# Kernel tuning notes

Hardware: AMD Instinct MI355X
Metric: run time of the kernel (lower is better)

Reference implementation:

```python
import jax, jax.numpy as jnp
import numpy as np

DECAY = 0.99
EPSILON = 1e-05
COMMITMENT_COST = 0.25
N_TOKENS = 8192   # B * h * w = 8 * 32 * 32
EMBED_DIM = 4096
VOCAB = 8192


def setup_inputs() -> dict:
    key = jax.random.key(0)
    k1, k2, k3 = jax.random.split(key, 3)
    return {
        "inputs": jax.random.normal(k1, (N_TOKENS, EMBED_DIM), dtype=jnp.float32),
        "embedding": jax.random.normal(k2, (VOCAB, EMBED_DIM), dtype=jnp.float32),
        "ema_w": jax.random.normal(k3, (VOCAB, EMBED_DIM), dtype=jnp.float32),
        "ema_cluster_size": jnp.zeros((VOCAB,), dtype=jnp.float32),
    }


def reference(inputs, embedding, ema_w, ema_cluster_size):
    n_tokens = inputs.shape[0]
    vocab = embedding.shape[0]
    distances = (jnp.sum(inputs * inputs, axis=1, keepdims=True)
                 + jnp.sum(embedding * embedding, axis=1)
                 - 2.0 * jnp.matmul(inputs, embedding.T))
    encoding_indices = jnp.argmin(distances, axis=1)            # [N]
    # one-hot @ embedding == gather of codebook rows
    quantized = embedding[encoding_indices]                      # [N, D]
    # sum of one-hot encodings over tokens == per-code counts
    counts = jax.ops.segment_sum(jnp.ones((n_tokens,), inputs.dtype),
                                 encoding_indices, num_segments=vocab)  # [V]
    # EMA cluster-size update with Laplace smoothing
    new_cluster_size = ema_cluster_size * DECAY + (1.0 - DECAY) * counts
    n = jnp.sum(new_cluster_size)
    new_cluster_size = (new_cluster_size + EPSILON) / (n + vocab * EPSILON) * n
    # dw = encodings.T @ flat_input == scatter-add of inputs per code
    dw = jax.ops.segment_sum(inputs, encoding_indices, num_segments=vocab)  # [V, D]
    new_ema_w = ema_w * DECAY + (1.0 - DECAY) * dw
    new_embedding = new_ema_w / new_cluster_size[:, None]
    # commitment loss (codebook side detached)
    e_latent_loss = jnp.mean((jax.lax.stop_gradient(quantized) - inputs) ** 2)
    loss = COMMITMENT_COST * e_latent_loss
    # straight-through estimator
    quantized_st = inputs + jax.lax.stop_gradient(quantized - inputs)
    avg_probs = counts / n_tokens
    perplexity = jnp.exp(-jnp.sum(avg_probs * jnp.log(avg_probs + 1e-10)))
    return (loss, quantized_st, perplexity, encoding_indices[:, None],
            new_cluster_size, new_ema_w, new_embedding)
```

## Files before the change

kernel.cpp:

```cpp
#include <hip/hip_runtime.h>
#include <hip/hip_fp16.h>
#include <stdint.h>

typedef _Float16 f16;
typedef float f32x4 __attribute__((ext_vector_type(4)));
typedef unsigned long long u64;
typedef long long i64;
typedef long long i64x2 __attribute__((ext_vector_type(2)));

#define N_TOK 8192
#define VOCAB 8192
#define DIM   4096
#define DELTA 64.0f

__device__ __forceinline__ void gload16(const void* g, void* l) {
    __builtin_amdgcn_global_load_lds(
        (const __attribute__((address_space(1))) unsigned int*)(uintptr_t)g,
        (__attribute__((address_space(3))) unsigned int*)(uintptr_t)l,
        16, 0, 0);
}

__device__ __forceinline__ float keyinv(unsigned k) {
    unsigned b = (k & 0x80000000u) ? (k ^ 0x80000000u) : ~k;
    return __uint_as_float(b);
}

__device__ __forceinline__ void ins2(u64& k1, u64& k2, u64 v) {
    if (v < k1) { k2 = k1; k1 = v; }
    else if (v < k2) { k2 = v; }
}

__global__ __launch_bounds__(256) void k_pack(const float* __restrict__ inputs,
                                              const float* __restrict__ embedding,
                                              char* __restrict__ apk, char* __restrict__ bpk,
                                              float* __restrict__ enorms,
                                              int* __restrict__ counts) {
    int b = blockIdx.x, t = threadIdx.x;
    bool isB = b >= N_TOK;
    int row = isB ? b - N_TOK : b;
    const float* src = (isB ? embedding : inputs) + (size_t)row * DIM;
    char* dst = (isB ? bpk : apk) + (size_t)row * DIM;
    double nrm = 0.0;
#pragma unroll
    for (int k = 0; k < 4; k++) {
        int d0 = t * 4 + 1024 * k;
        float4 v = *(const float4*)(src + d0);
        nrm += (double)v.x * v.x + (double)v.y * v.y
             + (double)v.z * v.z + (double)v.w * v.w;
        int packed = 0;
        packed = __builtin_amdgcn_cvt_pk_fp8_f32(v.x, v.y, packed, false);
        packed = __builtin_amdgcn_cvt_pk_fp8_f32(v.z, v.w, packed, true);
        int c = d0 & 127;
        int s8 = c >> 3, kk = s8 >> 2, g = s8 & 3;
        int q8 = ((kk & 2) << 2) | (g << 1) | (kk & 1);
        *(int*)(dst + (d0 & ~127) + (q8 << 3) + (c & 7)) = packed;
    }
    if (isB) {
        __shared__ double red[256];
        red[t] = nrm;
        __syncthreads();
        for (int off = 128; off > 0; off >>= 1) {
            if (t < off) red[t] += red[t + off];
            __syncthreads();
        }
        if (t == 0) {
            enorms[row] = (float)red[0];
            counts[row] = 0;
        }
    }
}

__global__ __launch_bounds__(512) void k_gemm(const char* __restrict__ apk,
                                              const char* __restrict__ bpk,
                                              const float* __restrict__ enorms,
                                              u64* __restrict__ cand) {
    extern __shared__ char lds[];
    int b = blockIdx.x;
    int x = b & 7, l = b >> 3;
    int bm = x * 4 + ((l >> 3) & 3);
    int bn = (l >> 5) * 8 + (l & 7);
    int tid = threadIdx.x;
    int lane = tid & 63, wid = tid >> 6;
    int wm = wid >> 2, wn = wid & 3;

    const char* srcs[8];
    unsigned lof[8];
#pragma unroll
    for (int e = 0; e < 8; e++) {
        int tile = e >> 2, q = e & 3;
        int s = q * 512 + tid;
        int r = s >> 3;
        int c16 = (s & 7) ^ (r & 7);
        int row = (tile ? bn : bm) * 256 + r;
        srcs[e] = (tile ? bpk : apk) + (size_t)row * DIM + c16 * 16;
        lof[e] = tile * 32768 + q * 8192 + wid * 1024;
    }

    f32x4 acc[8][4];
#pragma unroll
    for (int m = 0; m < 8; m++)
#pragma unroll
        for (int n = 0; n < 4; n++) acc[m][n] = (f32x4){0.f, 0.f, 0.f, 0.f};

    const int g = lane >> 4;
    const int ra = wm * 128 + (lane & 15);
    const int rb = wn * 64 + (lane & 15);

#define STAGE(buf) { _Pragma("unroll") for (int e = 0; e < 8; e++) { \
        gload16(srcs[e], &lds[(buf) * 65536u + lof[e]]); srcs[e] += 128; } }

    STAGE(0);

    for (int kt = 0; kt < 32; ++kt) {
        const unsigned cur = (kt & 1) ? 65536u : 0u;
        if (kt < 31) {
            STAGE((kt & 1) ^ 1);
            asm volatile("s_waitcnt vmcnt(8)" ::: "memory");
        } else {
            asm volatile("s_waitcnt vmcnt(0)" ::: "memory");
        }
        __builtin_amdgcn_sched_barrier(0);
        __builtin_amdgcn_s_barrier();
        __builtin_amdgcn_s_setprio(1);
#pragma unroll
        for (int h = 0; h < 2; h++) {
            i64x2 bv[4];
#pragma unroll
            for (int n = 0; n < 4; n++) {
                int r = rb + n * 16;
                bv[n] = *(const i64x2*)&lds[cur + 32768 + r * 128 + ((((h << 2) + g) ^ (r & 7)) << 4)];
            }
#pragma unroll
            for (int m = 0; m < 8; m++) {
                int r = ra + m * 16;
                i64x2 av = *(const i64x2*)&lds[cur + r * 128 + ((((h << 2) + g) ^ (r & 7)) << 4)];
#pragma unroll
                for (int n = 0; n < 4; n++) {
                    acc[m][n] = __builtin_amdgcn_mfma_f32_16x16x32_fp8_fp8(av[0], bv[n][0], acc[m][n], 0, 0, 0);
                    acc[m][n] = __builtin_amdgcn_mfma_f32_16x16x32_fp8_fp8(av[1], bv[n][1], acc[m][n], 0, 0, 0);
                }
            }
        }
        __builtin_amdgcn_s_setprio(0);
        __builtin_amdgcn_s_barrier();
    }
#undef STAGE

    float en[4];
    int colb = bn * 256 + wn * 64 + (lane & 15);
#pragma unroll
    for (int n = 0; n < 4; n++) en[n] = enorms[colb + n * 16];
#pragma unroll
    for (int m = 0; m < 8; m++) {
#pragma unroll
        for (int reg = 0; reg < 4; reg++) {
            u64 k1 = ~0ull, k2 = ~0ull;
#pragma unroll
            for (int n = 0; n < 4; n++) {
                float d = en[n] - 2.0f * acc[m][n][reg];
                unsigned bb = __float_as_uint(d);
                unsigned key = (bb & 0x80000000u) ? ~bb : (bb | 0x80000000u);
                ins2(k1, k2, ((u64)key << 32) | (unsigned)(colb + n * 16));
            }
#pragma unroll
            for (int msk = 1; msk < 16; msk <<= 1) {
                u64 o1 = __shfl_xor(k1, msk, 64);
                u64 o2 = __shfl_xor(k2, msk, 64);
                ins2(k1, k2, o1);
                ins2(k1, k2, o2);
            }
            if ((lane & 15) == 0) {
                int rowg = bm * 256 + wm * 128 + m * 16 + ((lane >> 4) << 2) + reg;
                size_t slot = ((size_t)rowg * 32 + bn) * 4 + wn;
                ulonglong2 v; v.x = k1; v.y = k2;
                *(ulonglong2*)&cand[slot * 2] = v;
            }
        }
    }
}

__global__ __launch_bounds__(256) void k_cand(const u64* __restrict__ cand,
                                              const float* __restrict__ enorms,
                                              const float* __restrict__ inputs,
                                              const float* __restrict__ embedding,
                                              float* __restrict__ o_idx,
                                              float* __restrict__ o_quant,
                                              float* __restrict__ partials,
                                              int* __restrict__ counts) {
    int tok = blockIdx.x, t = threadIdx.x;
    int lane = t & 63, w = t >> 6;
    __shared__ u64 redu[4];
    __shared__ float redf[4];
    __shared__ float pdot[64][4];
    __shared__ int clist[64];
    __shared__ int s_cnt;
    if (t == 0) s_cnt = 0;
    u64 e = cand[(size_t)tok * 256 + t];
    u64 v = e;
#pragma unroll
    for (int msk = 1; msk < 64; msk <<= 1) {
        u64 o = __shfl_xor(v, msk, 64);
        if (o < v) v = o;
    }
    if (lane == 0) redu[w] = v;
    __syncthreads();
    u64 m01 = redu[0] < redu[1] ? redu[0] : redu[1];
    u64 m23 = redu[2] < redu[3] ? redu[2] : redu[3];
    u64 mall = m01 < m23 ? m01 : m23;
    float dmin = keyinv((unsigned)(mall >> 32));
    float myd = keyinv((unsigned)(e >> 32));
    if (myd <= dmin + DELTA) {
        int p = atomicAdd(&s_cnt, 1);
        if (p < 64) clist[p] = (int)(unsigned)(e & 0xffffffffu);
    }
    __syncthreads();
    int nc = min(s_cnt, 64);

    const float* xrow = inputs + (size_t)tok * DIM;
    float4 xr4[4];
#pragma unroll
    for (int k = 0; k < 4; k++) xr4[k] = *(const float4*)(xrow + t * 4 + 1024 * k);

    for (int i = 0; i < nc; i++) {
        int c = clist[i];
        const float* erow = embedding + (size_t)c * DIM;
        float p = 0.f;
#pragma unroll
        for (int k = 0; k < 4; k++) {
            float4 e4 = *(const float4*)(erow + t * 4 + 1024 * k);
            p += xr4[k].x * e4.x + xr4[k].y * e4.y + xr4[k].z * e4.z + xr4[k].w * e4.w;
        }
#pragma unroll
        for (int msk = 1; msk < 64; msk <<= 1) p += __shfl_xor(p, msk, 64);
        if (lane == 0) pdot[i][w] = p;
    }
    __syncthreads();

    float best = 3.4e38f;
    int bcol = 0x7fffffff;
    for (int i = 0; i < nc; i++) {
        int c = clist[i];
        float dot = (pdot[i][0] + pdot[i][1]) + (pdot[i][2] + pdot[i][3]);
        float dist = enorms[c] - 2.0f * dot;
        if (dist < best || (dist == best && c < bcol)) { best = dist; bcol = c; }
    }
    const float* eb = embedding + (size_t)bcol * DIM;
    float* qrow = o_quant + (size_t)tok * DIM;
    float ls = 0.f;
#pragma unroll
    for (int k = 0; k < 4; k++) {
        int d = t * 4 + 1024 * k;
        float4 q4 = *(const float4*)(eb + d);
        qrow[d + 0] = q4.x; qrow[d + 1] = q4.y; qrow[d + 2] = q4.z; qrow[d + 3] = q4.w;
        float dx = q4.x - xr4[k].x, dy = q4.y - xr4[k].y;
        float dz = q4.z - xr4[k].z, dw = q4.w - xr4[k].w;
        ls += dx * dx + dy * dy + dz * dz + dw * dw;
    }
#pragma unroll
    for (int msk = 1; msk < 64; msk <<= 1) ls += __shfl_xor(ls, msk, 64);
    if (lane == 0) redf[w] = ls;
    __syncthreads();
    if (t == 0) {
        partials[tok] = (redf[0] + redf[1]) + (redf[2] + redf[3]);
        o_idx[tok] = (float)bcol;
        atomicAdd(&counts[bcol], 1);
    }
}

__global__ __launch_bounds__(1024) void k_cs(const int* __restrict__ counts,
                                             const float* __restrict__ ema_cs,
                                             float* __restrict__ o_ncs,
                                             float* __restrict__ o_perp) {
    __shared__ float red[1024];
    int t = threadIdx.x;
    float pre[8];
    float psum = 0.f, esum = 0.f;
#pragma unroll
    for (int k = 0; k < 8; k++) {
        int j = t * 8 + k;
        float c = (float)counts[j];
        float p = ema_cs[j] * 0.99f + 0.01f * c;
        pre[k] = p;
        psum += p;
        float ap = c * (1.0f / 8192.0f);
        esum += ap * logf(ap + 1e-10f);
    }
    red[t] = psum;
    __syncthreads();
    for (int off = 512; off > 0; off >>= 1) {
        if (t < off) red[t] += red[t + off];
        __syncthreads();
    }
    float n = red[0];
    __syncthreads();
    red[t] = esum;
    __syncthreads();
    for (int off = 512; off > 0; off >>= 1) {
        if (t < off) red[t] += red[t + off];
        __syncthreads();
    }
    if (t == 0) o_perp[0] = expf(-red[0]);
    float scale = n / (n + (float)VOCAB * 1e-5f);
#pragma unroll
    for (int k = 0; k < 8; k++) {
        int j = t * 8 + k;
        o_ncs[j] = (pre[k] + 1e-5f) * scale;
    }
}

__global__ __launch_bounds__(1024) void k_loss(const float* __restrict__ partials,
                                               float* __restrict__ o_loss) {
    __shared__ float red[1024];
    int t = threadIdx.x;
    float s = 0.f;
#pragma unroll
    for (int k = 0; k < 8; k++) s += partials[t * 8 + k];
    red[t] = s;
    __syncthreads();
    for (int off = 512; off > 0; off >>= 1) {
        if (t < off) red[t] += red[t + off];
        __syncthreads();
    }
    if (t == 0) o_loss[0] = 0.25f * red[0] / ((float)N_TOK * (float)DIM);
}

__global__ __launch_bounds__(256) void k_ema(const float* __restrict__ o_idx,
                                             const float* __restrict__ inputs,
                                             const float* __restrict__ ema_w,
                                             const float* __restrict__ o_ncs,
                                             float* __restrict__ o_neww,
                                             float* __restrict__ o_newemb) {
    int j = blockIdx.x, t = threadIdx.x;
    __shared__ int scan[256];
    __shared__ int list[256];
    __shared__ int s_total;
    int c = 0;
    for (int k = 0; k < 32; k++) {
        int tok = t * 32 + k;
        if ((int)o_idx[tok] == j) c++;
    }
    scan[t] = c;
    __syncthreads();
    for (int off = 1; off < 256; off <<= 1) {
        int add = (t >= off) ? scan[t - off] : 0;
        __syncthreads();
        scan[t] += add;
        __syncthreads();
    }
    int excl = scan[t] - c;
    if (t == 255) s_total = scan[255];
    __syncthreads();
    int pos = excl;
    for (int k = 0; k < 32; k++) {
        int tok = t * 32 + k;
        if ((int)o_idx[tok] == j && pos < 256) list[pos++] = tok;
    }
    __syncthreads();
    int total = s_total;
    float nc = o_ncs[j];
    size_t rowoff = (size_t)j * DIM;
#pragma unroll
    for (int k = 0; k < 4; k++) {
        int d = t * 4 + 1024 * k;
        float sx = 0.f, sy = 0.f, sz = 0.f, sw = 0.f;
        for (int q = 0; q < total; q++) {
            float4 v = *(const float4*)(inputs + (size_t)list[q] * DIM + d);
            sx += v.x; sy += v.y; sz += v.z; sw += v.w;
        }
        float4 w4 = *(const float4*)(ema_w + rowoff + d);
        float w0 = w4.x * 0.99f + 0.01f * sx;
        float w1 = w4.y * 0.99f + 0.01f * sy;
        float w2 = w4.z * 0.99f + 0.01f * sz;
        float w3 = w4.w * 0.99f + 0.01f * sw;
        o_neww[rowoff + d + 0] = w0; o_newemb[rowoff + d + 0] = w0 / nc;
        o_neww[rowoff + d + 1] = w1; o_newemb[rowoff + d + 1] = w1 / nc;
        o_neww[rowoff + d + 2] = w2; o_newemb[rowoff + d + 2] = w2 / nc;
        o_neww[rowoff + d + 3] = w3; o_newemb[rowoff + d + 3] = w3 / nc;
    }
}

extern "C" void kernel_launch(void* const* d_in, const int* in_sizes, int n_in,
                              void* d_out, int out_size, void* d_ws, size_t ws_size,
                              hipStream_t stream) {
    const float* inputs    = (const float*)d_in[0];
    const float* embedding = (const float*)d_in[1];
    const float* ema_w     = (const float*)d_in[2];
    const float* ema_cs    = (const float*)d_in[3];

    float* out = (float*)d_out;
    char* base = (char*)d_out;

    char* apk       = base;
    char* bpk       = base + 33554432;
    u64* cand       = (u64*)(base + 167772160);
    float* enorms   = (float*)(base + 184549376);
    int* counts     = (int*)(base + 184582144);
    float* partials = (float*)(base + 184614912);

    float* o_loss   = out;
    float* o_quant  = out + 1;
    float* o_perp   = out + 33554433;
    float* o_idx    = out + 33554434;
    float* o_ncs    = out + 33562626;
    float* o_neww   = out + 33570818;
    float* o_newemb = out + 67125250;

    k_pack<<<dim3(N_TOK + VOCAB), dim3(256), 0, stream>>>(inputs, embedding, apk, bpk,
                                                          enorms, counts);
    k_gemm<<<dim3(1024), dim3(512), 131072, stream>>>(apk, bpk, enorms, cand);
    k_cand<<<dim3(N_TOK), dim3(256), 0, stream>>>(cand, enorms, inputs, embedding,
                                                  o_idx, o_quant, partials, counts);
    k_cs<<<dim3(1), dim3(1024), 0, stream>>>(counts, ema_cs, o_ncs, o_perp);
    k_loss<<<dim3(1), dim3(1024), 0, stream>>>(partials, o_loss);
    k_ema<<<dim3(VOCAB), dim3(256), 0, stream>>>(o_idx, inputs, ema_w, o_ncs, o_neww, o_newemb);
}
```

Baseline: 1.415 ms.

## Switch FP8 GEMM to 16x16x128 scaled MFMA with interleaved staging schedule

Replaces the pairs of 16x16x32 fp8 MFMAs with the gfx950 mfma_scale 16x16x128 f8f6f4 instruction using unit scales, so each instruction consumes the full 128-byte K tile per row. The fp8 pack layout in the prep kernel is permuted to match the new operand ordering. The main loop is restructured into four quadrant phases that interleave LDS fragment loads, split global-to-LDS issues, and MFMA bursts with extra barriers. This aims to raise MFMA throughput and overlap copies with compute, at the cost of more barriers and a layout dependency between the kernels.

Measured after the change: 1.280 ms. 9.6% less time.

```diff
diff --git a/kernel.cpp b/kernel.cpp
--- a/kernel.cpp
+++ b/kernel.cpp
@@ -4,9 +4,9 @@
 
 typedef _Float16 f16;
 typedef float f32x4 __attribute__((ext_vector_type(4)));
+typedef int i32x4v __attribute__((ext_vector_type(4)));
+typedef int i32x8v __attribute__((ext_vector_type(8)));
 typedef unsigned long long u64;
-typedef long long i64;
-typedef long long i64x2 __attribute__((ext_vector_type(2)));
 
 #define N_TOK 8192
 #define VOCAB 8192
@@ -51,9 +51,9 @@
         packed = __builtin_amdgcn_cvt_pk_fp8_f32(v.x, v.y, packed, false);
         packed = __builtin_amdgcn_cvt_pk_fp8_f32(v.z, v.w, packed, true);
         int c = d0 & 127;
-        int s8 = c >> 3, kk = s8 >> 2, g = s8 & 3;
-        int q8 = ((kk & 2) << 2) | (g << 1) | (kk & 1);
-        *(int*)(dst + (d0 & ~127) + (q8 << 3) + (c & 7)) = packed;
+        int u = c >> 4;
+        int p = ((u & 1) << 2) | (u >> 1);
+        *(int*)(dst + (d0 & ~127) + (p << 4) + (c & 15)) = packed;
     }
     if (isB) {
         __shared__ double red[256];
@@ -103,61 +103,81 @@
         for (int n = 0; n < 4; n++) acc[m][n] = (f32x4){0.f, 0.f, 0.f, 0.f};
 
     const int g = lane >> 4;
-    const int ra = wm * 128 + (lane & 15);
-    const int rb = wn * 64 + (lane & 15);
-
-#define STAGE(buf) { _Pragma("unroll") for (int e = 0; e < 8; e++) { \
-        gload16(srcs[e], &lds[(buf) * 65536u + lof[e]]); srcs[e] += 128; } }
-
-    STAGE(0);
+    i32x8v a[4], b0[2], b1[2];
+
+#define ISSUE2(eA, eB) { gload16(srcs[eA], &lds[nbuf + lof[eA]]); srcs[eA] += 128; \
+                         gload16(srcs[eB], &lds[nbuf + lof[eB]]); srcs[eB] += 128; }
+#define LDA(mh) { _Pragma("unroll") for (int m = 0; m < 4; m++) { \
+        int r = wm * 128 + (mh) * 64 + m * 16 + (lane & 15); \
+        i32x4v lo = *(const i32x4v*)&lds[cur + r * 128 + ((g ^ (r & 7)) << 4)]; \
+        i32x4v hi = *(const i32x4v*)&lds[cur + r * 128 + (((4 + g) ^ (r & 7)) << 4)]; \
+        a[m] = __builtin_shufflevector(lo, hi, 0, 1, 2, 3, 4, 5, 6, 7); } }
+#define LDB(bb, nh) { _Pragma("unroll") for (int n = 0; n < 2; n++) { \
+        int r = wn * 64 + (nh) * 32 + n * 16 + (lane & 15); \
+        i32x4v lo = *(const i32x4v*)&lds[cur + 32768 + r * 128 + ((g ^ (r & 7)) << 4)]; \
+        i32x4v hi = *(const i32x4v*)&lds[cur + 32768 + r * 128 + (((4 + g) ^ (r & 7)) << 4)]; \
+        bb[n] = __builtin_shufflevector(lo, hi, 0, 1, 2, 3, 4, 5, 6, 7); } }
+#define QUAD(mh, nh, bb) { _Pragma("unroll") for (int m = 0; m < 4; m++) \
+        _Pragma("unroll") for (int n = 0; n < 2; n++) \
+        acc[(mh) * 4 + m][(nh) * 2 + n] = __builtin_amdgcn_mfma_scale_f32_16x16x128_f8f6f4( \
+            a[m], bb[n], acc[(mh) * 4 + m][(nh) * 2 + n], 0, 0, \
+            0, 0x7F7F7F7F, 0, 0x7F7F7F7F); }
+#define BARRIER() __builtin_amdgcn_s_barrier()
+#define LGKM0() { asm volatile("s_waitcnt lgkmcnt(0)" ::: "memory"); \
+                  __builtin_amdgcn_sched_barrier(0); }
+
+    {
+        const unsigned nbuf = 0u;
+        ISSUE2(0, 1); ISSUE2(2, 3); ISSUE2(4, 5); ISSUE2(6, 7);
+    }
 
     for (int kt = 0; kt < 32; ++kt) {
         const unsigned cur = (kt & 1) ? 65536u : 0u;
+        const unsigned nbuf = cur ^ 65536u;
         if (kt < 31) {
-            STAGE((kt & 1) ^ 1);
-            asm volatile("s_waitcnt vmcnt(8)" ::: "memory");
+            ISSUE2(0, 1);
+            asm volatile("s_waitcnt vmcnt(2)" ::: "memory");
         } else {
             asm volatile("s_waitcnt vmcnt(0)" ::: "memory");
         }
         __builtin_amdgcn_sched_barrier(0);
-        __builtin_amdgcn_s_barrier();
-        __builtin_amdgcn_s_setprio(1);
-#pragma unroll
-        for (int h = 0; h < 2; h++) {
-            i64x2 bv[4];
-#pragma unroll
-            for (int n = 0; n < 4; n++) {
-                int r = rb + n * 16;
-                bv[n] = *(const i64x2*)&lds[cur + 32768 + r * 128 + ((((h << 2) + g) ^ (r & 7)) << 4)];
-            }
-#pragma unroll
-            for (int m = 0; m < 8; m++) {
-                int r = ra + m * 16;
-                i64x2 av = *(const i64x2*)&lds[cur + r * 128 + ((((h << 2) + g) ^ (r & 7)) << 4)];
-#pragma unroll
-                for (int n = 0; n < 4; n++) {
-                    acc[m][n] = __builtin_amdgcn_mfma_f32_16x16x32_fp8_fp8(av[0], bv[n][0], acc[m][n], 0, 0, 0);
-                    acc[m][n] = __builtin_amdgcn_mfma_f32_16x16x32_fp8_fp8(av[1], bv[n][1], acc[m][n], 0, 0, 0);
-                }
-            }
-        }
-        __builtin_amdgcn_s_setprio(0);
-        __builtin_amdgcn_s_barrier();
-    }
-#undef STAGE
+        BARRIER();
+        LDA(0); LDB(b0, 0);
+        if (kt < 31) ISSUE2(2, 3);
+        BARRIER(); LGKM0();
+        __builtin_amdgcn_s_setprio(1); QUAD(0, 0, b0); __builtin_amdgcn_s_setprio(0);
+        BARRIER();
+        LDB(b1, 1);
+        if (kt < 31) ISSUE2(4, 5);
+        BARRIER(); LGKM0();
+        __builtin_amdgcn_s_setprio(1); QUAD(0, 1, b1); __builtin_amdgcn_s_setprio(0);
+        BARRIER();
+        LDA(1);
+        if (kt < 31) ISSUE2(6, 7);
+        BARRIER(); LGKM0();
+        __builtin_amdgcn_s_setprio(1); QUAD(1, 0, b0); __builtin_amdgcn_s_setprio(0);
+        BARRIER();
+        __builtin_amdgcn_s_setprio(1); QUAD(1, 1, b1); __builtin_amdgcn_s_setprio(0);
+    }
+#undef ISSUE2
+#undef LDA
+#undef LDB
+#undef QUAD
+#undef BARRIER
+#undef LGKM0
 
     float en[4];
     int colb = bn * 256 + wn * 64 + (lane & 15);
 #pragma unroll
     for (int n = 0; n < 4; n++) en[n] = enorms[colb + n * 16];
 #pragma unroll
-    for (int m = 0; m < 8; m++) {
+    for (int M = 0; M < 8; M++) {
 #pragma unroll
         for (int reg = 0; reg < 4; reg++) {
             u64 k1 = ~0ull, k2 = ~0ull;
 #pragma unroll
             for (int n = 0; n < 4; n++) {
-                float d = en[n] - 2.0f * acc[m][n][reg];
+                float d = en[n] - 2.0f * acc[M][n][reg];
                 unsigned bb = __float_as_uint(d);
                 unsigned key = (bb & 0x80000000u) ? ~bb : (bb | 0x80000000u);
                 ins2(k1, k2, ((u64)key << 32) | (unsigned)(colb + n * 16));
@@ -170,7 +190,7 @@
                 ins2(k1, k2, o2);
             }
             if ((lane & 15) == 0) {
-                int rowg = bm * 256 + wm * 128 + m * 16 + ((lane >> 4) << 2) + reg;
+                int rowg = bm * 256 + wm * 128 + M * 16 + ((lane >> 4) << 2) + reg;
                 size_t slot = ((size_t)rowg * 32 + bn) * 4 + wn;
                 ulonglong2 v; v.x = k1; v.y = k2;
                 *(ulonglong2*)&cand[slot * 2] = v;
```
